# Kernel tuning notes

Hardware: AMD Instinct MI355X
Metric: run time of the kernel (lower is better)

The kernel has to match this reference:

```python
import math
import jax, jax.numpy as jnp
import numpy as np

EMBED_DIM = 512
NUM_HEADS = 8
HEAD_DIM = EMBED_DIM // NUM_HEADS
NUM_EDGE_TYPES = 10
N = 2048  # nodes
B = 1


def setup_inputs() -> dict:
    key = jax.random.key(0)
    ks = jax.random.split(key, 8)
    s = 1.0 / math.sqrt(EMBED_DIM)
    return {
        "query": jax.random.normal(ks[0], (N, B, EMBED_DIM), jnp.float32),
        "key": jax.random.normal(ks[1], (N, B, EMBED_DIM), jnp.float32),
        "value": jax.random.normal(ks[2], (N, B, EMBED_DIM), jnp.float32),
        "edge_id_mat": jax.random.randint(ks[3], (N, N), 0, NUM_EDGE_TYPES, jnp.int32),
        "in_proj_weight": jax.random.normal(ks[4], (3 * EMBED_DIM, EMBED_DIM), jnp.float32) * s,
        "in_proj_bias": jnp.zeros((3 * EMBED_DIM,), jnp.float32),
        "out_proj_weight": jax.random.normal(ks[5], (EMBED_DIM, EMBED_DIM), jnp.float32) * s,
        "out_proj_bias": jnp.zeros((EMBED_DIM,), jnp.float32),
        "edge_embs_K": jax.random.normal(ks[6], (NUM_EDGE_TYPES, HEAD_DIM), jnp.float32),
    }


def reference(query, key, value, edge_id_mat, in_proj_weight, in_proj_bias,
              out_proj_weight, out_proj_bias, edge_embs_K):
    L, Bsz, E = query.shape
    H, hd = NUM_HEADS, HEAD_DIM
    w_q, w_k, w_v = jnp.split(in_proj_weight, 3, axis=0)
    b_q, b_k, b_v = jnp.split(in_proj_bias, 3)
    q = query @ w_q.T + b_q   # (L, B, E)
    k = key @ w_k.T + b_k
    v = value @ w_v.T + b_v

    def split_heads(x):
        # (L, B, E) -> (B*H, L, hd)  (matches torch view(L, B*H, hd).transpose(0,1))
        return x.reshape(L, Bsz * H, hd).transpose(1, 0, 2)

    q = split_heads(q) / math.sqrt(hd)  # torch scales by sqrt(E=head_dim)
    k = split_heads(k)
    v = split_heads(v)

    attn = jnp.einsum('bnd,bmd->bnm', q, k)  # (B*H, L, L)

    # edge-type score bias: edge_attn[b,i,j] = q[b,i,:] . edge_embs_K[edge_id_mat[i,j], :]
    # computed efficiently as per-type scores then a gather (avoids (L,L,hd) tensor)
    type_scores = jnp.einsum('bnd,td->bnt', q, edge_embs_K)  # (B*H, L, T)
    idx = jnp.broadcast_to(edge_id_mat[None, :, :], attn.shape)
    edge_attn = jnp.take_along_axis(type_scores, idx, axis=2)  # (B*H, L, L)
    attn = jax.nn.softmax(attn + edge_attn, axis=-1)

    out = jnp.einsum('bnm,bmd->bnd', attn, v)           # (B*H, L, hd)
    out = out.transpose(1, 0, 2).reshape(L, Bsz, E)      # (L, B, E)
    out = out @ out_proj_weight.T + out_proj_bias
    return out
```

## Files before the change

### kernel.cpp

```cpp
#include <hip/hip_runtime.h>
#include <hip/hip_bf16.h>

#define NHEAD 8
#define SEQ   2048
#define HD    64
#define EMB   512
#define NTYPE 10
#define JSPLIT 2

typedef unsigned short u16;
typedef __attribute__((ext_vector_type(8))) short short8;
typedef __attribute__((ext_vector_type(4))) float float4v;

union F8 { short8 v; uint4 u4; u16 us[8]; };

__device__ __forceinline__ float bf2f(u16 u){
  union { unsigned u; float f; } w; w.u = ((unsigned)u) << 16; return w.f;
}
__device__ __forceinline__ u16 f2bf(float f){
  union { float f; unsigned u; } w; w.f = f;
  unsigned u = w.u;
  u += 0x7fffu + ((u >> 16) & 1u);
  return (u16)(u >> 16);
}
__device__ __forceinline__ unsigned pk2(float a, float b){
  return (unsigned)f2bf(a) | ((unsigned)f2bf(b) << 16);
}

__device__ __forceinline__ void gload_lds16(const u16* g, u16* l){
  __builtin_amdgcn_global_load_lds(
      (const __attribute__((address_space(1))) unsigned int*)g,
      (__attribute__((address_space(3))) unsigned int*)l, 16, 0, 0);
}

__global__ __launch_bounds__(256) void prep_kernel(
    const float* __restrict__ q, const float* __restrict__ k, const float* __restrict__ v,
    const float* __restrict__ ipw, const float* __restrict__ opw,
    const int* __restrict__ eid,
    u16* __restrict__ Abf, u16* __restrict__ Wbf, u16* __restrict__ OWbf,
    unsigned* __restrict__ eidp)
{
  const int gid = blockIdx.x * 256 + threadIdx.x;
  if (blockIdx.x < 2048) {
    const int e8 = gid * 8;
    const float* src; u16* dst; int off;
    if      (e8 < 1048576) { src = q;   dst = Abf;            off = e8; }
    else if (e8 < 2097152) { src = k;   dst = Abf + 1048576;  off = e8 - 1048576; }
    else if (e8 < 3145728) { src = v;   dst = Abf + 2097152;  off = e8 - 2097152; }
    else if (e8 < 3932160) { src = ipw; dst = Wbf;            off = e8 - 3145728; }
    else                   { src = opw; dst = OWbf;           off = e8 - 3932160; }
    float4 a = *(const float4*)(src + off);
    float4 b = *(const float4*)(src + off + 4);
    uint4 p; p.x = pk2(a.x, a.y); p.y = pk2(a.z, a.w);
             p.z = pk2(b.x, b.y); p.w = pk2(b.z, b.w);
    *(uint4*)(dst + off) = p;
  } else {
    const int i = gid - 524288;
    int4 vv = ((const int4*)eid)[i];
    eidp[i] = (unsigned)(vv.x & 0xff) | ((unsigned)(vv.y & 0xff) << 8) |
              ((unsigned)(vv.z & 0xff) << 16) | ((unsigned)(vv.w & 0xff) << 24);
  }
}

template<int WNF, int MODE>
__global__ __launch_bounds__(256) void gemm_bt(
    const u16* __restrict__ Aall, const u16* __restrict__ Bw,
    const float* __restrict__ bias,
    u16* __restrict__ Qs, u16* __restrict__ Kb, u16* __restrict__ Vb,
    float* __restrict__ outF)
{
  constexpr int BN = WNF * 32;
  constexpr int K  = 512;
  __shared__ u16 lds[128 * 32 + BN * 32];
  u16* As = lds;
  u16* Bs = lds + 128 * 32;

  const int t = threadIdx.x, w = t >> 6, lane = t & 63, lr = lane & 15, lg = lane >> 4;
  const int n0 = blockIdx.x * BN;
  const int m0 = blockIdx.y * 128;
  const int wm = w >> 1, wn = w & 1;

  int z = 0;
  const u16* A = Aall;
  if (MODE == 0) { z = n0 >> 9; A = Aall + (size_t)z * (2048 * 512); }

  float4v acc[4][WNF];
#pragma unroll
  for (int mi = 0; mi < 4; mi++)
#pragma unroll
    for (int ni = 0; ni < WNF; ni++) acc[mi][ni] = (float4v){0.f, 0.f, 0.f, 0.f};

  const int rb = lane >> 2, kb = (lane & 3) * 8;

  for (int k0 = 0; k0 < K; k0 += 32) {
    __syncthreads();
#pragma unroll
    for (int c = 0; c < 2; c++) {
      const int ci = w * 2 + c;
      gload_lds16(A + (size_t)(m0 + ci * 16 + rb) * K + k0 + kb, As + ci * 512);
    }
#pragma unroll
    for (int c = 0; c < WNF / 2; c++) {
      const int ci = w * (WNF / 2) + c;
      gload_lds16(Bw + (size_t)(n0 + ci * 16 + rb) * K + k0 + kb, Bs + ci * 512);
    }
    __syncthreads();

    F8 af[4], bfr[WNF];
#pragma unroll
    for (int mi = 0; mi < 4; mi++)
      af[mi].u4 = *(const uint4*)(As + (wm * 64 + mi * 16 + lr) * 32 + lg * 8);
#pragma unroll
    for (int ni = 0; ni < WNF; ni++)
      bfr[ni].u4 = *(const uint4*)(Bs + (wn * (BN / 2) + ni * 16 + lr) * 32 + lg * 8);
#pragma unroll
    for (int mi = 0; mi < 4; mi++)
#pragma unroll
      for (int ni = 0; ni < WNF; ni++)
        acc[mi][ni] = __builtin_amdgcn_mfma_f32_16x16x32_bf16(af[mi].v, bfr[ni].v, acc[mi][ni], 0, 0, 0);
  }

  if (MODE == 0) {
    u16* O = (z == 0) ? Qs : ((z == 1) ? Kb : Vb);
    const float scale = (z == 0) ? 0.125f : 1.0f;
#pragma unroll
    for (int mi = 0; mi < 4; mi++) {
#pragma unroll
      for (int ni = 0; ni < WNF; ni++) {
        const int n = n0 + wn * (BN / 2) + ni * 16 + lr;
        const int e = n & 511, h = e >> 6, d = e & 63;
        const float bb = bias[n];
        const int mb = m0 + wm * 64 + mi * 16 + lg * 4;
        if (z < 2) {
#pragma unroll
          for (int r = 0; r < 4; r++)
            O[((size_t)h * SEQ + mb + r) * HD + d] = f2bf((acc[mi][ni][r] + bb) * scale);
        } else {
          ushort4 pk;
          pk.x = f2bf(acc[mi][ni][0] + bb); pk.y = f2bf(acc[mi][ni][1] + bb);
          pk.z = f2bf(acc[mi][ni][2] + bb); pk.w = f2bf(acc[mi][ni][3] + bb);
          *(ushort4*)(O + ((size_t)(h * HD + d)) * SEQ + mb) = pk;
        }
      }
    }
  } else {
#pragma unroll
    for (int mi = 0; mi < 4; mi++) {
#pragma unroll
      for (int ni = 0; ni < WNF; ni++) {
        const int n = n0 + wn * (BN / 2) + ni * 16 + lr;
        const float bb = bias[n];
        const int mb = m0 + wm * 64 + mi * 16 + lg * 4;
#pragma unroll
        for (int r = 0; r < 4; r++)
          outF[(size_t)(mb + r) * EMB + n] = acc[mi][ni][r] + bb;
      }
    }
  }
}

__global__ __launch_bounds__(256) void attn_kernel(
    const u16* __restrict__ Qs, const u16* __restrict__ Kb, const u16* __restrict__ Vb,
    const unsigned char* __restrict__ eidp, const float* __restrict__ EK,
    float* __restrict__ Upart, float* __restrict__ mpart, float* __restrict__ lpart)
{
  __shared__ u16 Kt[64][72];
  __shared__ u16 Vt[64][72];
  __shared__ u16 Pl[4][16][72];
  __shared__ unsigned char eidt[64][64];
  __shared__ float tsl[64][13];
  __shared__ float ekl[NTYPE][64];
  __shared__ float mrow[64], lrow[64], frow[64];

  const int t = threadIdx.x;
  const int wave = t >> 6, lane = t & 63, lr = lane & 15, lg = lane >> 4;
  const int i0 = blockIdx.x * 64;
  const int h  = blockIdx.y;
  const int z  = blockIdx.z;

  for (int i = t; i < NTYPE * 64; i += 256) ekl[i >> 6][i & 63] = EK[i];
  if (t < 64) { mrow[t] = -1e30f; lrow[t] = 0.f; }
  __syncthreads();

  {
    const int row = t >> 2, tt = t & 3;
    const u16* qr = Qs + ((size_t)h * SEQ + i0 + row) * HD;
    float a0 = 0.f, a1 = 0.f, a2 = 0.f;
    for (int d0 = 0; d0 < HD; d0 += 8) {
      uint4 qq = *(const uint4*)(qr + d0);
      const u16* qu = (const u16*)&qq;
#pragma unroll
      for (int e = 0; e < 8; e++) {
        float qf = bf2f(qu[e]);
        a0 += qf * ekl[tt][d0 + e];
        a1 += qf * ekl[tt + 4][d0 + e];
        a2 += qf * ekl[(tt < 2) ? (tt + 8) : 8][d0 + e];
      }
    }
    tsl[row][tt] = a0; tsl[row][tt + 4] = a1;
    if (tt < 2) tsl[row][tt + 8] = a2;
  }

  F8 qf[2];
#pragma unroll
  for (int kc = 0; kc < 2; kc++)
    qf[kc].u4 = *(const uint4*)(Qs + ((size_t)h * SEQ + i0 + wave * 16 + lr) * HD + kc * 32 + lg * 8);

  float4v ao[4];
#pragma unroll
  for (int d = 0; d < 4; d++) ao[d] = (float4v){0.f, 0.f, 0.f, 0.f};

  const int srow = t >> 2, sdc = (t & 3) * 16;
  const int sec = sdc ^ (((t >> 4) & 3) << 4);
  const int jbase = z * (SEQ / JSPLIT);
  const int NT = (SEQ / JSPLIT) / 64;

  uint4 kp0, kp1, vp0, vp1, ep0;
  {
    const u16* kp = Kb + ((size_t)h * SEQ + jbase + srow) * HD + sdc;
    kp0 = *(const uint4*)kp; kp1 = *(const uint4*)(kp + 8);
    const u16* vp = Vb + ((size_t)(h * HD + srow)) * SEQ + jbase + sdc;
    vp0 = *(const uint4*)vp; vp1 = *(const uint4*)(vp + 8);
    ep0 = *(const uint4*)(eidp + (size_t)(i0 + srow) * SEQ + jbase + sdc);
    *(uint4*)&Kt[srow][sdc] = kp0; *(uint4*)&Kt[srow][sdc + 8] = kp1;
    *(uint4*)&Vt[srow][sdc] = vp0; *(uint4*)&Vt[srow][sdc + 8] = vp1;
    *(uint4*)&eidt[srow][sec] = ep0;
  }

  for (int jt = 0; jt < NT; jt++) {
    __syncthreads();

    if (jt + 1 < NT) {
      const int jn = jbase + (jt + 1) * 64;
      const u16* kp = Kb + ((size_t)h * SEQ + jn + srow) * HD + sdc;
      kp0 = *(const uint4*)kp; kp1 = *(const uint4*)(kp + 8);
      const u16* vp = Vb + ((size_t)(h * HD + srow)) * SEQ + jn + sdc;
      vp0 = *(const uint4*)vp; vp1 = *(const uint4*)(vp + 8);
      ep0 = *(const uint4*)(eidp + (size_t)(i0 + srow) * SEQ + jn + sdc);
    }

    float4v sacc[4];
#pragma unroll
    for (int c = 0; c < 4; c++) sacc[c] = (float4v){0.f, 0.f, 0.f, 0.f};
#pragma unroll
    for (int kc = 0; kc < 2; kc++) {
#pragma unroll
      for (int c = 0; c < 4; c++) {
        F8 kf; kf.u4 = *(const uint4*)&Kt[c * 16 + lr][kc * 32 + lg * 8];
        sacc[c] = __builtin_amdgcn_mfma_f32_16x16x32_bf16(qf[kc].v, kf.v, sacc[c], 0, 0, 0);
      }
    }

    float pv_[4][4];
    float rmax[4] = {-1e30f, -1e30f, -1e30f, -1e30f};
#pragma unroll
    for (int c = 0; c < 4; c++) {
      const int ec = ((c ^ lg) << 4) + lr;
#pragma unroll
      for (int r = 0; r < 4; r++) {
        const int row = wave * 16 + lg * 4 + r;
        float s = sacc[c][r] + tsl[row][eidt[row][ec]];
        pv_[c][r] = s;
        rmax[r] = fmaxf(rmax[r], s);
      }
    }
#pragma unroll
    for (int mm = 1; mm < 16; mm <<= 1) {
#pragma unroll
      for (int r = 0; r < 4; r++) rmax[r] = fmaxf(rmax[r], __shfl_xor(rmax[r], mm));
    }
    float mnew[4], fct[4], rsum[4] = {0.f, 0.f, 0.f, 0.f};
#pragma unroll
    for (int r = 0; r < 4; r++) {
      const int row = wave * 16 + lg * 4 + r;
      const float mo = mrow[row];
      mnew[r] = fmaxf(mo, rmax[r]);
      fct[r] = __expf(mo - mnew[r]);
    }
#pragma unroll
    for (int c = 0; c < 4; c++) {
#pragma unroll
      for (int r = 0; r < 4; r++) {
        float p = __expf(pv_[c][r] - mnew[r]);
        pv_[c][r] = p;
        rsum[r] += p;
      }
    }
#pragma unroll
    for (int mm = 1; mm < 16; mm <<= 1) {
#pragma unroll
      for (int r = 0; r < 4; r++) rsum[r] += __shfl_xor(rsum[r], mm);
    }
    if (lr == 0) {
#pragma unroll
      for (int r = 0; r < 4; r++) {
        const int row = wave * 16 + lg * 4 + r;
        mrow[row] = mnew[r];
        lrow[row] = lrow[row] * fct[r] + rsum[r];
        frow[row] = fct[r];
      }
    }
#pragma unroll
    for (int c = 0; c < 4; c++) {
#pragma unroll
      for (int r = 0; r < 4; r++)
        Pl[wave][lg * 4 + r][c * 16 + lr] = f2bf(pv_[c][r]);
    }
    const float fo = frow[wave * 16 + lr];
#pragma unroll
    for (int d = 0; d < 4; d++) {
#pragma unroll
      for (int r = 0; r < 4; r++) ao[d][r] *= fo;
    }
#pragma unroll
    for (int kc = 0; kc < 2; kc++) {
      F8 pf; pf.u4 = *(const uint4*)&Pl[wave][lr][kc * 32 + lg * 8];
#pragma unroll
      for (int db = 0; db < 4; db++) {
        F8 vf; vf.u4 = *(const uint4*)&Vt[db * 16 + lr][kc * 32 + lg * 8];
        ao[db] = __builtin_amdgcn_mfma_f32_16x16x32_bf16(vf.v, pf.v, ao[db], 0, 0, 0);
      }
    }

    __syncthreads();
    if (jt + 1 < NT) {
      *(uint4*)&Kt[srow][sdc] = kp0; *(uint4*)&Kt[srow][sdc + 8] = kp1;
      *(uint4*)&Vt[srow][sdc] = vp0; *(uint4*)&Vt[srow][sdc + 8] = vp1;
      *(uint4*)&eidt[srow][sec] = ep0;
    }
  }

  {
    const size_t base = (((size_t)z * NHEAD + h) * SEQ + i0) * HD;
#pragma unroll
    for (int db = 0; db < 4; db++) {
#pragma unroll
      for (int r = 0; r < 4; r++) {
        const int d = db * 16 + lg * 4 + r;
        const int n = wave * 16 + lr;
        Upart[base + (size_t)n * HD + d] = ao[db][r];
      }
    }
    __syncthreads();
    if (t < 64) {
      mpart[((size_t)z * NHEAD + h) * SEQ + i0 + t] = mrow[t];
      lpart[((size_t)z * NHEAD + h) * SEQ + i0 + t] = lrow[t];
    }
  }
}

__global__ __launch_bounds__(256) void combine_kernel(
    const float* __restrict__ Upart, const float* __restrict__ mpart,
    const float* __restrict__ lpart, u16* __restrict__ AObf)
{
  const int rid = blockIdx.x * 4 + (threadIdx.x >> 6);
  const int d = threadIdx.x & 63;
  float mm[JSPLIT];
  float M = -1e30f;
#pragma unroll
  for (int zz = 0; zz < JSPLIT; zz++) {
    mm[zz] = mpart[(size_t)zz * NHEAD * SEQ + rid];
    M = fmaxf(M, mm[zz]);
  }
  float Ls = 0.f, U = 0.f;
#pragma unroll
  for (int zz = 0; zz < JSPLIT; zz++) {
    const float w = __expf(mm[zz] - M);
    Ls += w * lpart[(size_t)zz * NHEAD * SEQ + rid];
    U  += w * Upart[((size_t)zz * NHEAD * SEQ + rid) * HD + d];
  }
  const int hh = rid >> 11;
  const int n = rid & (SEQ - 1);
  AObf[(size_t)n * EMB + hh * HD + d] = f2bf(U / Ls);
}

extern "C" void kernel_launch(void* const* d_in, const int* in_sizes, int n_in,
                              void* d_out, int out_size, void* d_ws, size_t ws_size,
                              hipStream_t stream)
{
  const float* query = (const float*)d_in[0];
  const float* key_  = (const float*)d_in[1];
  const float* value = (const float*)d_in[2];
  const int*   eid   = (const int*)d_in[3];
  const float* ipw   = (const float*)d_in[4];
  const float* ipb   = (const float*)d_in[5];
  const float* opw   = (const float*)d_in[6];
  const float* opb   = (const float*)d_in[7];
  const float* ek    = (const float*)d_in[8];
  float* out = (float*)d_out;

  char* ws = (char*)d_ws;
  u16* Abf  = (u16*)ws;            ws += (size_t)3 * SEQ * EMB * 2;
  u16* Wbf  = (u16*)ws;            ws += (size_t)3 * EMB * EMB * 2;
  u16* OWbf = (u16*)ws;            ws += (size_t)EMB * EMB * 2;
  u16* Qs = (u16*)ws;              ws += (size_t)NHEAD * SEQ * HD * 2;
  u16* Kb = (u16*)ws;              ws += (size_t)NHEAD * SEQ * HD * 2;
  u16* Vb = (u16*)ws;              ws += (size_t)NHEAD * SEQ * HD * 2;
  unsigned char* eidp = (unsigned char*)ws; ws += (size_t)SEQ * SEQ;
  float* Upart = (float*)ws;       ws += (size_t)JSPLIT * NHEAD * SEQ * HD * 4;
  float* mpart = (float*)ws;       ws += (size_t)JSPLIT * NHEAD * SEQ * 4;
  float* lpart = (float*)ws;       ws += (size_t)JSPLIT * NHEAD * SEQ * 4;
  u16* AObf    = (u16*)ws;         ws += (size_t)SEQ * EMB * 2;

  prep_kernel<<<dim3(6144), dim3(256), 0, stream>>>(
      query, key_, value, ipw, opw, eid, Abf, Wbf, OWbf, (unsigned*)eidp);
  gemm_bt<4, 0><<<dim3(3 * EMB / 128, SEQ / 128), dim3(256), 0, stream>>>(
      Abf, Wbf, ipb, Qs, Kb, Vb, nullptr);
  attn_kernel<<<dim3(SEQ / 64, NHEAD, JSPLIT), dim3(256), 0, stream>>>(
      Qs, Kb, Vb, eidp, ek, Upart, mpart, lpart);
  combine_kernel<<<dim3(NHEAD * SEQ / 4), dim3(256), 0, stream>>>(Upart, mpart, lpart, AObf);
  gemm_bt<2, 1><<<dim3(EMB / 64, SEQ / 128), dim3(256), 0, stream>>>(
      AObf, OWbf, opb, nullptr, nullptr, nullptr, out);
}
```

Before: 162.3 us.

## Fuse bf16 conversion into QKV GEMM and split-combine into output projection

```diff
diff --git a/kernel.cpp b/kernel.cpp
--- a/kernel.cpp
+++ b/kernel.cpp
@@ -8,6 +8,11 @@
 #define NTYPE 10
 #define JSPLIT 2
 
+#define QKV_NT (3 * EMB / 64)
+#define QKV_MT (SEQ / 64)
+#define QKV_BLOCKS (QKV_NT * QKV_MT)
+#define PACK_BLOCKS (SEQ * SEQ / 4 / 256)
+
 typedef unsigned short u16;
 typedef __attribute__((ext_vector_type(8))) short short8;
 typedef __attribute__((ext_vector_type(4))) float float4v;
@@ -26,134 +31,95 @@
 __device__ __forceinline__ unsigned pk2(float a, float b){
   return (unsigned)f2bf(a) | ((unsigned)f2bf(b) << 16);
 }
-
-__device__ __forceinline__ void gload_lds16(const u16* g, u16* l){
-  __builtin_amdgcn_global_load_lds(
-      (const __attribute__((address_space(1))) unsigned int*)g,
-      (__attribute__((address_space(3))) unsigned int*)l, 16, 0, 0);
-}
-
-__global__ __launch_bounds__(256) void prep_kernel(
+__device__ __forceinline__ uint4 pk8(float4 a, float4 b){
+  uint4 p; p.x = pk2(a.x, a.y); p.y = pk2(a.z, a.w);
+           p.z = pk2(b.x, b.y); p.w = pk2(b.z, b.w);
+  return p;
+}
+
+__global__ __launch_bounds__(256) void fused_prep_gemm(
     const float* __restrict__ q, const float* __restrict__ k, const float* __restrict__ v,
-    const float* __restrict__ ipw, const float* __restrict__ opw,
-    const int* __restrict__ eid,
-    u16* __restrict__ Abf, u16* __restrict__ Wbf, u16* __restrict__ OWbf,
+    const float* __restrict__ ipw, const float* __restrict__ ipb, const int* __restrict__ eid,
+    u16* __restrict__ Qs, u16* __restrict__ Kb, u16* __restrict__ Vb,
     unsigned* __restrict__ eidp)
 {
-  const int gid = blockIdx.x * 256 + threadIdx.x;
-  if (blockIdx.x < 2048) {
-    const int e8 = gid * 8;
-    const float* src; u16* dst; int off;
-    if      (e8 < 1048576) { src = q;   dst = Abf;            off = e8; }
-    else if (e8 < 2097152) { src = k;   dst = Abf + 1048576;  off = e8 - 1048576; }
-    else if (e8 < 3145728) { src = v;   dst = Abf + 2097152;  off = e8 - 2097152; }
-    else if (e8 < 3932160) { src = ipw; dst = Wbf;            off = e8 - 3145728; }
-    else                   { src = opw; dst = OWbf;           off = e8 - 3932160; }
-    float4 a = *(const float4*)(src + off);
-    float4 b = *(const float4*)(src + off + 4);
-    uint4 p; p.x = pk2(a.x, a.y); p.y = pk2(a.z, a.w);
-             p.z = pk2(b.x, b.y); p.w = pk2(b.z, b.w);
-    *(uint4*)(dst + off) = p;
-  } else {
-    const int i = gid - 524288;
+  const int b = blockIdx.x;
+  const int t = threadIdx.x;
+
+  if (b >= QKV_BLOCKS) {
+    const int i = (b - QKV_BLOCKS) * 256 + t;
     int4 vv = ((const int4*)eid)[i];
     eidp[i] = (unsigned)(vv.x & 0xff) | ((unsigned)(vv.y & 0xff) << 8) |
               ((unsigned)(vv.z & 0xff) << 16) | ((unsigned)(vv.w & 0xff) << 24);
-  }
-}
-
-template<int WNF, int MODE>
-__global__ __launch_bounds__(256) void gemm_bt(
-    const u16* __restrict__ Aall, const u16* __restrict__ Bw,
-    const float* __restrict__ bias,
-    u16* __restrict__ Qs, u16* __restrict__ Kb, u16* __restrict__ Vb,
-    float* __restrict__ outF)
-{
-  constexpr int BN = WNF * 32;
-  constexpr int K  = 512;
-  __shared__ u16 lds[128 * 32 + BN * 32];
-  u16* As = lds;
-  u16* Bs = lds + 128 * 32;
-
-  const int t = threadIdx.x, w = t >> 6, lane = t & 63, lr = lane & 15, lg = lane >> 4;
-  const int n0 = blockIdx.x * BN;
-  const int m0 = blockIdx.y * 128;
+    return;
+  }
+
+  __shared__ u16 As[64][40];
+  __shared__ u16 Bs[64][40];
+
+  const int nt = b % QKV_NT, mt = b / QKV_NT;
+  const int n0 = nt * 64, m0 = mt * 64;
+  const int z = n0 >> 9;
+  const float* A = (z == 0) ? q : (z == 1) ? k : v;
+  const float scale = (z == 0) ? 0.125f : 1.0f;
+
+  const int w = t >> 6, lane = t & 63, lr = lane & 15, lg = lane >> 4;
   const int wm = w >> 1, wn = w & 1;
-
-  int z = 0;
-  const u16* A = Aall;
-  if (MODE == 0) { z = n0 >> 9; A = Aall + (size_t)z * (2048 * 512); }
-
-  float4v acc[4][WNF];
-#pragma unroll
-  for (int mi = 0; mi < 4; mi++)
-#pragma unroll
-    for (int ni = 0; ni < WNF; ni++) acc[mi][ni] = (float4v){0.f, 0.f, 0.f, 0.f};
-
-  const int rb = lane >> 2, kb = (lane & 3) * 8;
-
-  for (int k0 = 0; k0 < K; k0 += 32) {
-    __syncthreads();
-#pragma unroll
-    for (int c = 0; c < 2; c++) {
-      const int ci = w * 2 + c;
-      gload_lds16(A + (size_t)(m0 + ci * 16 + rb) * K + k0 + kb, As + ci * 512);
-    }
-#pragma unroll
-    for (int c = 0; c < WNF / 2; c++) {
-      const int ci = w * (WNF / 2) + c;
-      gload_lds16(Bw + (size_t)(n0 + ci * 16 + rb) * K + k0 + kb, Bs + ci * 512);
-    }
-    __syncthreads();
-
-    F8 af[4], bfr[WNF];
-#pragma unroll
-    for (int mi = 0; mi < 4; mi++)
-      af[mi].u4 = *(const uint4*)(As + (wm * 64 + mi * 16 + lr) * 32 + lg * 8);
-#pragma unroll
-    for (int ni = 0; ni < WNF; ni++)
-      bfr[ni].u4 = *(const uint4*)(Bs + (wn * (BN / 2) + ni * 16 + lr) * 32 + lg * 8);
-#pragma unroll
-    for (int mi = 0; mi < 4; mi++)
-#pragma unroll
-      for (int ni = 0; ni < WNF; ni++)
-        acc[mi][ni] = __builtin_amdgcn_mfma_f32_16x16x32_bf16(af[mi].v, bfr[ni].v, acc[mi][ni], 0, 0, 0);
-  }
-
-  if (MODE == 0) {
-    u16* O = (z == 0) ? Qs : ((z == 1) ? Kb : Vb);
-    const float scale = (z == 0) ? 0.125f : 1.0f;
-#pragma unroll
-    for (int mi = 0; mi < 4; mi++) {
-#pragma unroll
-      for (int ni = 0; ni < WNF; ni++) {
-        const int n = n0 + wn * (BN / 2) + ni * 16 + lr;
-        const int e = n & 511, h = e >> 6, d = e & 63;
-        const float bb = bias[n];
-        const int mb = m0 + wm * 64 + mi * 16 + lg * 4;
-        if (z < 2) {
-#pragma unroll
-          for (int r = 0; r < 4; r++)
-            O[((size_t)h * SEQ + mb + r) * HD + d] = f2bf((acc[mi][ni][r] + bb) * scale);
-        } else {
-          ushort4 pk;
-          pk.x = f2bf(acc[mi][ni][0] + bb); pk.y = f2bf(acc[mi][ni][1] + bb);
-          pk.z = f2bf(acc[mi][ni][2] + bb); pk.w = f2bf(acc[mi][ni][3] + bb);
-          *(ushort4*)(O + ((size_t)(h * HD + d)) * SEQ + mb) = pk;
-        }
-      }
-    }
-  } else {
-#pragma unroll
-    for (int mi = 0; mi < 4; mi++) {
-#pragma unroll
-      for (int ni = 0; ni < WNF; ni++) {
-        const int n = n0 + wn * (BN / 2) + ni * 16 + lr;
-        const float bb = bias[n];
-        const int mb = m0 + wm * 64 + mi * 16 + lg * 4;
+  const int srow = t >> 2, kb = (t & 3) * 8;
+
+  float4v acc[2][2];
+#pragma unroll
+  for (int mi = 0; mi < 2; mi++)
+#pragma unroll
+    for (int ni = 0; ni < 2; ni++) acc[mi][ni] = (float4v){0.f, 0.f, 0.f, 0.f};
+
+  const float* pa = A   + (size_t)(m0 + srow) * EMB + kb;
+  const float* pw = ipw + (size_t)(n0 + srow) * EMB + kb;
+
+  float4 a0 = *(const float4*)pa, a1 = *(const float4*)(pa + 4);
+  float4 b0 = *(const float4*)pw, b1 = *(const float4*)(pw + 4);
+
+  for (int k0 = 0; k0 < EMB; k0 += 32) {
+    *(uint4*)&As[srow][kb] = pk8(a0, a1);
+    *(uint4*)&Bs[srow][kb] = pk8(b0, b1);
+    __syncthreads();
+    if (k0 + 32 < EMB) {
+      a0 = *(const float4*)(pa + k0 + 32); a1 = *(const float4*)(pa + k0 + 36);
+      b0 = *(const float4*)(pw + k0 + 32); b1 = *(const float4*)(pw + k0 + 36);
+    }
+    F8 af[2], bf_[2];
+#pragma unroll
+    for (int mi = 0; mi < 2; mi++)
+      af[mi].u4 = *(const uint4*)&As[wm * 32 + mi * 16 + lr][lg * 8];
+#pragma unroll
+    for (int ni = 0; ni < 2; ni++)
+      bf_[ni].u4 = *(const uint4*)&Bs[wn * 32 + ni * 16 + lr][lg * 8];
+#pragma unroll
+    for (int mi = 0; mi < 2; mi++)
+#pragma unroll
+      for (int ni = 0; ni < 2; ni++)
+        acc[mi][ni] = __builtin_amdgcn_mfma_f32_16x16x32_bf16(af[mi].v, bf_[ni].v, acc[mi][ni], 0, 0, 0);
+    __syncthreads();
+  }
+
+  u16* O = (z == 0) ? Qs : ((z == 1) ? Kb : Vb);
+#pragma unroll
+  for (int mi = 0; mi < 2; mi++) {
+#pragma unroll
+    for (int ni = 0; ni < 2; ni++) {
+      const int n = n0 + wn * 32 + ni * 16 + lr;
+      const int e = n & 511, h = e >> 6, d = e & 63;
+      const float bb = ipb[n];
+      const int mb = m0 + wm * 32 + mi * 16 + lg * 4;
+      if (z < 2) {
 #pragma unroll
         for (int r = 0; r < 4; r++)
-          outF[(size_t)(mb + r) * EMB + n] = acc[mi][ni][r] + bb;
+          O[((size_t)h * SEQ + mb + r) * HD + d] = f2bf((acc[mi][ni][r] + bb) * scale);
+      } else {
+        ushort4 pk;
+        pk.x = f2bf(acc[mi][ni][0] + bb); pk.y = f2bf(acc[mi][ni][1] + bb);
+        pk.z = f2bf(acc[mi][ni][2] + bb); pk.w = f2bf(acc[mi][ni][3] + bb);
+        *(ushort4*)(O + ((size_t)(h * HD + d)) * SEQ + mb) = pk;
       }
     }
   }
@@ -242,6 +208,7 @@
     float4v sacc[4];
 #pragma unroll
     for (int c = 0; c < 4; c++) sacc[c] = (float4v){0.f, 0.f, 0.f, 0.f};
+    __builtin_amdgcn_s_setprio(1);
 #pragma unroll
     for (int kc = 0; kc < 2; kc++) {
 #pragma unroll
@@ -250,6 +217,7 @@
         sacc[c] = __builtin_amdgcn_mfma_f32_16x16x32_bf16(qf[kc].v, kf.v, sacc[c], 0, 0, 0);
       }
     }
+    __builtin_amdgcn_s_setprio(0);
 
     float pv_[4][4];
     float rmax[4] = {-1e30f, -1e30f, -1e30f, -1e30f};
@@ -312,6 +280,7 @@
 #pragma unroll
       for (int r = 0; r < 4; r++) ao[d][r] *= fo;
     }
+    __builtin_amdgcn_s_setprio(1);
 #pragma unroll
     for (int kc = 0; kc < 2; kc++) {
       F8 pf; pf.u4 = *(const uint4*)&Pl[wave][lr][kc * 32 + lg * 8];
@@ -321,6 +290,7 @@
         ao[db] = __builtin_amdgcn_mfma_f32_16x16x32_bf16(vf.v, pf.v, ao[db], 0, 0, 0);
       }
     }
+    __builtin_amdgcn_s_setprio(0);
 
     __syncthreads();
     if (jt + 1 < NT) {
@@ -349,29 +319,99 @@
   }
 }
 
-__global__ __launch_bounds__(256) void combine_kernel(
+__global__ __launch_bounds__(256) void combine_outproj(
     const float* __restrict__ Upart, const float* __restrict__ mpart,
-    const float* __restrict__ lpart, u16* __restrict__ AObf)
+    const float* __restrict__ lpart, const float* __restrict__ opw,
+    const float* __restrict__ opb, float* __restrict__ out)
 {
-  const int rid = blockIdx.x * 4 + (threadIdx.x >> 6);
-  const int d = threadIdx.x & 63;
-  float mm[JSPLIT];
-  float M = -1e30f;
-#pragma unroll
-  for (int zz = 0; zz < JSPLIT; zz++) {
-    mm[zz] = mpart[(size_t)zz * NHEAD * SEQ + rid];
-    M = fmaxf(M, mm[zz]);
-  }
-  float Ls = 0.f, U = 0.f;
-#pragma unroll
-  for (int zz = 0; zz < JSPLIT; zz++) {
-    const float w = __expf(mm[zz] - M);
-    Ls += w * lpart[(size_t)zz * NHEAD * SEQ + rid];
-    U  += w * Upart[((size_t)zz * NHEAD * SEQ + rid) * HD + d];
-  }
-  const int hh = rid >> 11;
-  const int n = rid & (SEQ - 1);
-  AObf[(size_t)n * EMB + hh * HD + d] = f2bf(U / Ls);
+  __shared__ u16 As[64][40];
+  __shared__ u16 Bs[64][40];
+  __shared__ float cw0[NHEAD][64], cw1[NHEAD][64], cwi[NHEAD][64];
+
+  const int t = threadIdx.x;
+  const int n0 = blockIdx.x * 64;
+  const int m0 = blockIdx.y * 64;
+
+  for (int idx = t; idx < NHEAD * 64; idx += 256) {
+    const int hh = idx >> 6, nl = idx & 63;
+    const int gn = m0 + nl;
+    const float mA = mpart[((size_t)0 * NHEAD + hh) * SEQ + gn];
+    const float mB = mpart[((size_t)1 * NHEAD + hh) * SEQ + gn];
+    const float M = fmaxf(mA, mB);
+    const float w0 = __expf(mA - M), w1 = __expf(mB - M);
+    const float Ls = w0 * lpart[((size_t)0 * NHEAD + hh) * SEQ + gn] +
+                     w1 * lpart[((size_t)1 * NHEAD + hh) * SEQ + gn];
+    cw0[hh][nl] = w0; cw1[hh][nl] = w1; cwi[hh][nl] = 1.0f / Ls;
+  }
+  __syncthreads();
+
+  const int w = t >> 6, lane = t & 63, lr = lane & 15, lg = lane >> 4;
+  const int wm = w >> 1, wn = w & 1;
+  const int srow = t >> 2, kb = (t & 3) * 8;
+
+  float4v acc[2][2];
+#pragma unroll
+  for (int mi = 0; mi < 2; mi++)
+#pragma unroll
+    for (int ni = 0; ni < 2; ni++) acc[mi][ni] = (float4v){0.f, 0.f, 0.f, 0.f};
+
+  const float* pw = opw + (size_t)(n0 + srow) * EMB + kb;
+
+  int hcur = kb >> 6, dcur = kb & 63;
+  const float* pu0 = Upart + (((size_t)0 * NHEAD + hcur) * SEQ + m0 + srow) * HD + dcur;
+  const float* pu1 = Upart + (((size_t)1 * NHEAD + hcur) * SEQ + m0 + srow) * HD + dcur;
+  float4 u00 = *(const float4*)pu0, u01 = *(const float4*)(pu0 + 4);
+  float4 u10 = *(const float4*)pu1, u11 = *(const float4*)(pu1 + 4);
+  float4 b0 = *(const float4*)pw, b1 = *(const float4*)(pw + 4);
+
+  for (int k0 = 0; k0 < EMB; k0 += 32) {
+    {
+      const float w0 = cw0[hcur][srow], w1 = cw1[hcur][srow], wi = cwi[hcur][srow];
+      float4 c0, c1;
+      c0.x = (u00.x * w0 + u10.x * w1) * wi; c0.y = (u00.y * w0 + u10.y * w1) * wi;
+      c0.z = (u00.z * w0 + u10.z * w1) * wi; c0.w = (u00.w * w0 + u10.w * w1) * wi;
+      c1.x = (u01.x * w0 + u11.x * w1) * wi; c1.y = (u01.y * w0 + u11.y * w1) * wi;
+      c1.z = (u01.z * w0 + u11.z * w1) * wi; c1.w = (u01.w * w0 + u11.w * w1) * wi;
+      *(uint4*)&As[srow][kb] = pk8(c0, c1);
+      *(uint4*)&Bs[srow][kb] = pk8(b0, b1);
+    }
+    __syncthreads();
+    if (k0 + 32 < EMB) {
+      const int e = k0 + 32 + kb;
+      hcur = e >> 6; dcur = e & 63;
+      const float* q0 = Upart + (((size_t)0 * NHEAD + hcur) * SEQ + m0 + srow) * HD + dcur;
+      const float* q1 = Upart + (((size_t)1 * NHEAD + hcur) * SEQ + m0 + srow) * HD + dcur;
+      u00 = *(const float4*)q0; u01 = *(const float4*)(q0 + 4);
+      u10 = *(const float4*)q1; u11 = *(const float4*)(q1 + 4);
+      b0 = *(const float4*)(pw + k0 + 32); b1 = *(const float4*)(pw + k0 + 36);
+    }
+    F8 af[2], bf_[2];
+#pragma unroll
+    for (int mi = 0; mi < 2; mi++)
+      af[mi].u4 = *(const uint4*)&As[wm * 32 + mi * 16 + lr][lg * 8];
+#pragma unroll
+    for (int ni = 0; ni < 2; ni++)
+      bf_[ni].u4 = *(const uint4*)&Bs[wn * 32 + ni * 16 + lr][lg * 8];
+#pragma unroll
+    for (int mi = 0; mi < 2; mi++)
+#pragma unroll
+      for (int ni = 0; ni < 2; ni++)
+        acc[mi][ni] = __builtin_amdgcn_mfma_f32_16x16x32_bf16(af[mi].v, bf_[ni].v, acc[mi][ni], 0, 0, 0);
+    __syncthreads();
+  }
+
+#pragma unroll
+  for (int mi = 0; mi < 2; mi++) {
+#pragma unroll
+    for (int ni = 0; ni < 2; ni++) {
+      const int n = n0 + wn * 32 + ni * 16 + lr;
+      const float bb = opb[n];
+      const int mb = m0 + wm * 32 + mi * 16 + lg * 4;
+#pragma unroll
+      for (int r = 0; r < 4; r++)
+        out[(size_t)(mb + r) * EMB + n] = acc[mi][ni][r] + bb;
+    }
+  }
 }
 
 extern "C" void kernel_launch(void* const* d_in, const int* in_sizes, int n_in,
@@ -390,9 +430,6 @@
   float* out = (float*)d_out;
 
   char* ws = (char*)d_ws;
-  u16* Abf  = (u16*)ws;            ws += (size_t)3 * SEQ * EMB * 2;
-  u16* Wbf  = (u16*)ws;            ws += (size_t)3 * EMB * EMB * 2;
-  u16* OWbf = (u16*)ws;            ws += (size_t)EMB * EMB * 2;
   u16* Qs = (u16*)ws;              ws += (size_t)NHEAD * SEQ * HD * 2;
   u16* Kb = (u16*)ws;              ws += (size_t)NHEAD * SEQ * HD * 2;
   u16* Vb = (u16*)ws;              ws += (size_t)NHEAD * SEQ * HD * 2;
@@ -400,15 +437,11 @@
   float* Upart = (float*)ws;       ws += (size_t)JSPLIT * NHEAD * SEQ * HD * 4;
   float* mpart = (float*)ws;       ws += (size_t)JSPLIT * NHEAD * SEQ * 4;
   float* lpart = (float*)ws;       ws += (size_t)JSPLIT * NHEAD * SEQ * 4;
-  u16* AObf    = (u16*)ws;         ws += (size_t)SEQ * EMB * 2;
-
-  prep_kernel<<<dim3(6144), dim3(256), 0, stream>>>(
-      query, key_, value, ipw, opw, eid, Abf, Wbf, OWbf, (unsigned*)eidp);
-  gemm_bt<4, 0><<<dim3(3 * EMB / 128, SEQ / 128), dim3(256), 0, stream>>>(
-      Abf, Wbf, ipb, Qs, Kb, Vb, nullptr);
+
+  fused_prep_gemm<<<dim3(QKV_BLOCKS + PACK_BLOCKS), dim3(256), 0, stream>>>(
+      query, key_, value, ipw, ipb, eid, Qs, Kb, Vb, (unsigned*)eidp);
   attn_kernel<<<dim3(SEQ / 64, NHEAD, JSPLIT), dim3(256), 0, stream>>>(
       Qs, Kb, Vb, eidp, ek, Upart, mpart, lpart);
-  combine_kernel<<<dim3(NHEAD * SEQ / 4), dim3(256), 0, stream>>>(Upart, mpart, lpart, AObf);
-  gemm_bt<2, 1><<<dim3(EMB / 64, SEQ / 128), dim3(256), 0, stream>>>(
-      AObf, OWbf, opb, nullptr, nullptr, nullptr, out);
-}
+  combine_outproj<<<dim3(EMB / 64, SEQ / 64), dim3(256), 0, stream>>>(
+      Upart, mpart, lpart, opw, opb, out);
+}
```

New measurement: 165.2 us. Within noise of the previous version (+1.8%).
